# Kernel tuning notes

Measured on AMD Instinct MI355X. Metric: run time of the kernel, lower is better.

## Reference

```python
import jax, jax.numpy as jnp
import numpy as np

NQ = 10
C64 = jnp.complex64

# ---- gate matrices (built from traced fp32 params) ----

def u3(t, p, d):
    c = jnp.cos(t * 0.5).astype(C64)
    s = jnp.sin(t * 0.5).astype(C64)
    ep = jnp.exp(1j * p.astype(C64))
    ed = jnp.exp(1j * d.astype(C64))
    return jnp.stack([jnp.stack([c, -ed * s]), jnp.stack([ep * s, ep * ed * c])])

def ry(t):
    c = jnp.cos(t * 0.5).astype(C64)
    s = jnp.sin(t * 0.5).astype(C64)
    return jnp.stack([jnp.stack([c, -s]), jnp.stack([s, c])])

def rz(t):
    e = jnp.exp(-0.5j * t.astype(C64))
    ep = jnp.exp(0.5j * t.astype(C64))
    return jnp.diag(jnp.stack([e, ep]))

def rx(t):
    c = jnp.cos(t * 0.5).astype(C64)
    s = jnp.sin(t * 0.5).astype(C64)
    return jnp.stack([jnp.stack([c, -1j * s]), jnp.stack([-1j * s, c])])

def crz(t):
    one = jnp.ones((), C64)
    return jnp.diag(jnp.stack([one, one, jnp.exp(-0.5j * t.astype(C64)), jnp.exp(0.5j * t.astype(C64))]))

def crx(t):
    return jnp.eye(4, dtype=C64).at[2:, 2:].set(rx(t))

X = jnp.array([[0, 1], [1, 0]], dtype=C64)
CNOT = jnp.array([[1, 0, 0, 0], [0, 1, 0, 0], [0, 0, 0, 1], [0, 0, 1, 0]], dtype=C64)

# ---- gate application on state of shape (B, 2,...,2) ----

def ap1(st, U, w):
    ax = 1 + w
    s = jnp.moveaxis(st, ax, -1)
    s = s @ U.T
    return jnp.moveaxis(s, -1, ax)

def ap2(st, U, a, b):
    s = jnp.moveaxis(st, (1 + a, 1 + b), (-2, -1))
    sh = s.shape
    s = s.reshape(sh[:-2] + (4,)) @ U.T
    return jnp.moveaxis(s.reshape(sh), (-2, -1), (1 + a, 1 + b))

def conv_block(st, w, a, b):
    st = ap1(st, u3(w[0], w[1], w[2]), a)
    st = ap1(st, u3(w[3], w[4], w[5]), b)
    st = ap2(st, CNOT, a, b)
    st = ap1(st, ry(w[6]), a)
    st = ap1(st, rz(w[7]), b)
    st = ap2(st, CNOT, b, a)
    st = ap1(st, ry(w[8]), a)
    st = ap2(st, CNOT, a, b)
    st = ap1(st, u3(w[9], w[10], w[11]), a)
    st = ap1(st, u3(w[12], w[13], w[14]), b)
    return st

def pool_block(st, p, c, t):
    st = ap2(st, crz(p[0]), c, t)
    st = ap1(st, X, c)
    st = ap2(st, crx(p[1]), c, t)
    return st

def zexp(st, w):
    p = jnp.abs(st) ** 2  # fp32
    axes = tuple(ax for ax in range(1, NQ + 1) if ax != 1 + w)
    pz = p.sum(axis=axes)  # (B, 2)
    return pz[:, 0] - pz[:, 1]


def setup_inputs() -> dict:
    key = jax.random.key(0)
    ks = jax.random.split(key, 6)
    two_pi = 2.0 * np.pi
    return {
        "x": jax.random.normal(ks[0], (16384, 1024), dtype=jnp.float32),
        "weights_conv1": jax.random.uniform(ks[1], (10, 15), jnp.float32) * two_pi,
        "weights_conv2": jax.random.uniform(ks[2], (4, 15), jnp.float32) * two_pi,
        "weights_pool1": jax.random.uniform(ks[3], (5, 2), jnp.float32) * two_pi,
        "weights_pool2": jax.random.uniform(ks[4], (2, 2), jnp.float32) * two_pi,
        "weights_fc": jax.random.uniform(ks[5], (3,), jnp.float32) * two_pi,
    }


def reference(x, weights_conv1, weights_conv2, weights_pool1, weights_pool2, weights_fc):
    B = x.shape[0]
    # AmplitudeEmbedding with normalize=True (input already 1024-dim, no padding)
    nrm = jnp.linalg.norm(x, axis=1, keepdims=True)
    st = (x / nrm).astype(C64).reshape((B,) + (2,) * NQ)
    # conv layer 1: even pairs, odd pairs, wraparound (0, 9) reusing row 7
    for i in range(0, NQ, 2):
        st = conv_block(st, weights_conv1[i], i, i + 1)
    for i in range(1, NQ - 1, 2):
        st = conv_block(st, weights_conv1[i], i, i + 1)
    st = conv_block(st, weights_conv1[7], 0, NQ - 1)
    # pool layer 1
    for idx, i in enumerate(range(0, NQ, 2)):
        st = pool_block(st, weights_pool1[idx], i + 1, i)
    # conv layer 2 (stride-2 wires)
    for idx, i in enumerate(range(0, NQ - 2, 2)):
        st = conv_block(st, weights_conv2[idx], i, i + 2)
    # pool layer 2
    for idx, i in enumerate(range(0, NQ - 2, 4)):
        st = pool_block(st, weights_pool2[idx], i + 2, i)
    # fully-connected entanglers + RX rotations
    st = ap2(st, CNOT, 0, 4)
    st = ap2(st, CNOT, 2, 4)
    st = ap2(st, CNOT, 4, 0)
    st = ap1(st, rx(weights_fc[0]), 0)
    st = ap1(st, rx(weights_fc[1]), 2)
    st = ap1(st, rx(weights_fc[2]), 4)
    return jnp.stack([zexp(st, 0), zexp(st, 2)], axis=-1)  # (B, 2)
```

## Files before the change

kernel.cpp:

```cpp
#include <hip/hip_runtime.h>


typedef _Float16 f16;
typedef f16 f16x8 __attribute__((ext_vector_type(8)));
typedef f16 f16x4 __attribute__((ext_vector_type(4)));
typedef f16 f16x2 __attribute__((ext_vector_type(2)));
typedef float f32x4 __attribute__((ext_vector_type(4)));

__device__ inline float2 cmul(float2 a, float2 b) {
    return make_float2(a.x * b.x - a.y * b.y, a.x * b.y + a.y * b.x);
}
__device__ inline float2 cadd(float2 a, float2 b) {
    return make_float2(a.x + b.x, a.y + b.y);
}

struct M2 { float2 m[4]; };

__device__ inline M2 m2_u3(float t, float p, float d) {
    float c = cosf(0.5f * t), s = sinf(0.5f * t);
    float2 ep = make_float2(cosf(p), sinf(p));
    float2 ed = make_float2(cosf(d), sinf(d));
    M2 U;
    U.m[0] = make_float2(c, 0.f);
    U.m[1] = make_float2(-ed.x * s, -ed.y * s);
    U.m[2] = make_float2(ep.x * s, ep.y * s);
    float2 epd = cmul(ep, ed);
    U.m[3] = make_float2(epd.x * c, epd.y * c);
    return U;
}
__device__ inline M2 m2_ry(float t) {
    float c = cosf(0.5f * t), s = sinf(0.5f * t);
    M2 U;
    U.m[0] = make_float2(c, 0.f);  U.m[1] = make_float2(-s, 0.f);
    U.m[2] = make_float2(s, 0.f);  U.m[3] = make_float2(c, 0.f);
    return U;
}
__device__ inline M2 m2_rz(float t) {
    float c = cosf(0.5f * t), s = sinf(0.5f * t);
    M2 U;
    U.m[0] = make_float2(c, -s); U.m[1] = make_float2(0.f, 0.f);
    U.m[2] = make_float2(0.f, 0.f); U.m[3] = make_float2(c, s);
    return U;
}
__device__ inline M2 m2_rx(float t) {
    float c = cosf(0.5f * t), s = sinf(0.5f * t);
    M2 U;
    U.m[0] = make_float2(c, 0.f);   U.m[1] = make_float2(0.f, -s);
    U.m[2] = make_float2(0.f, -s);  U.m[3] = make_float2(c, 0.f);
    return U;
}

__device__ inline void ap2x2(float2& x, float2& y, const M2& U) {
    float2 nx = cadd(cmul(U.m[0], x), cmul(U.m[1], y));
    float2 ny = cadd(cmul(U.m[2], x), cmul(U.m[3], y));
    x = nx; y = ny;
}
__device__ inline void apA(float2 v[4], const M2& U) { ap2x2(v[0], v[2], U); ap2x2(v[1], v[3], U); }
__device__ inline void apB(float2 v[4], const M2& U) { ap2x2(v[0], v[1], U); ap2x2(v[2], v[3], U); }
__device__ inline void swapv(float2& a, float2& b) { float2 t = a; a = b; b = t; }

__device__ inline void conv_col(const float* w, float2 v[4]) {
    apA(v, m2_u3(w[0], w[1], w[2]));
    apB(v, m2_u3(w[3], w[4], w[5]));
    swapv(v[2], v[3]);
    apA(v, m2_ry(w[6]));
    apB(v, m2_rz(w[7]));
    swapv(v[1], v[3]);
    apA(v, m2_ry(w[8]));
    swapv(v[2], v[3]);
    apA(v, m2_u3(w[9], w[10], w[11]));
    apB(v, m2_u3(w[12], w[13], w[14]));
}
__device__ inline void pool_col(const float* p, float2 v[4]) {
    {
        float c = cosf(0.5f * p[0]), s = sinf(0.5f * p[0]);
        v[2] = cmul(v[2], make_float2(c, -s));
        v[3] = cmul(v[3], make_float2(c, s));
    }
    swapv(v[0], v[2]); swapv(v[1], v[3]);
    {
        M2 U = m2_rx(p[1]);
        ap2x2(v[2], v[3], U);
    }
}

__global__ void build_gates(const float* wc1, const float* wc2,
                            const float* wp1, const float* wp2,
                            const float* wfc, int2* gp, float2* gm) {
    const int t = threadIdx.x;
    const int n = t >> 2, c = t & 3;
    if (blockIdx.x != 0 || n >= 27) return;

    float2 v[4];
    for (int i = 0; i < 4; i++) v[i] = make_float2(0.f, 0.f);
    v[c] = make_float2(1.f, 0.f);

    int a, b;
    if (n < 5)        { int i = 2*n;       a = i;   b = i+1; conv_col(wc1 + 15*i, v); }
    else if (n < 9)   { int i = 2*(n-5)+1; a = i;   b = i+1; conv_col(wc1 + 15*i, v); }
    else if (n == 9)  { a = 0; b = 9;      conv_col(wc1 + 105, v); }
    else if (n < 15)  { int idx = n-10, i = 2*idx; a = i+1; b = i; pool_col(wp1 + 2*idx, v); }
    else if (n < 19)  { int idx = n-15, i = 2*idx; a = i; b = i+2; conv_col(wc2 + 15*idx, v); }
    else if (n == 19) { a = 2; b = 0;      pool_col(wp2 + 0, v); }
    else if (n == 20) { a = 6; b = 4;      pool_col(wp2 + 2, v); }
    else if (n <= 23) {
        a = (n == 21) ? 0 : (n == 22) ? 2 : 4;
        b = (n == 23) ? 0 : 4;
        swapv(v[2], v[3]);
    } else {
        a = (n == 24) ? 0 : (n == 25) ? 2 : 4;
        b = a + 1;
        apA(v, m2_rx(wfc[n - 24]));
    }
    if (c == 0) gp[n] = make_int2(9 - a, 9 - b);
    for (int i = 0; i < 4; i++) gm[n * 16 + i * 4 + c] = v[i];
}

#define SIM_BLOCKS 256
#define NORM_BLOCKS 2048

__global__ __launch_bounds__(256) void prep(const float* __restrict__ X,
                                            const int2* __restrict__ gp,
                                            const float2* __restrict__ gm,
                                            float* __restrict__ nrm2,
                                            f16* __restrict__ Xh,
                                            f16* __restrict__ BTh,
                                            float* __restrict__ out) {
    __shared__ float2 st[4][1025];
    const int bid = blockIdx.x;

    if (bid >= SIM_BLOCKS) {
        const int nb = bid - SIM_BLOCKS;
        const int w = threadIdx.x >> 6, l = threadIdx.x & 63;
        if (threadIdx.x < 16) out[nb * 16 + threadIdx.x] = 1.0f;
#pragma unroll
        for (int r = 0; r < 2; r++) {
            const int row = nb * 8 + w * 2 + r;
            const float4* xr = (const float4*)(X + (size_t)row * 1024);
            float s = 0.f;
#pragma unroll
            for (int ch = 0; ch < 4; ch++) {
                float4 v = xr[ch * 64 + l];
                f16x4 h;
                h[0] = (f16)v.x; h[1] = (f16)v.y; h[2] = (f16)v.z; h[3] = (f16)v.w;
                *(f16x4*)(Xh + (size_t)row * 1024 + (ch * 64 + l) * 4) = h;
                s += v.x * v.x + v.y * v.y + v.z * v.z + v.w * v.w;
            }
#pragma unroll
            for (int off = 32; off >= 1; off >>= 1) s += __shfl_xor(s, off, 64);
            if (l == 0) nrm2[row] = s;
        }
        return;
    }

    const int sb = bid;
    const int t0 = (sb & 7) * 128 + (sb >> 3) * 4;

    for (int i = threadIdx.x; i < 1024; i += 256) {
#pragma unroll
        for (int c = 0; c < 4; c++)
            st[c][i] = make_float2((i == t0 + c) ? 1.f : 0.f, 0.f);
    }
    __syncthreads();

    for (int g = 0; g < 27; g++) {
        const int2 p = gp[g];
        float2 m[16];
#pragma unroll
        for (int i = 0; i < 16; i++) m[i] = gm[g * 16 + i];
        const int p1 = p.x, p2 = p.y;
        const int lo = min(p1, p2), hi = max(p1, p2);
        const int q = threadIdx.x;
        const int m1 = (1 << lo) - 1;
        int tt = (q & m1) | ((q & ~m1) << 1);
        const int m2m = (1 << hi) - 1;
        const int i0 = (tt & m2m) | ((tt & ~m2m) << 1);
        int idx[4];
        for (int ga = 0; ga < 2; ga++)
            for (int gb = 0; gb < 2; gb++)
                idx[2 * ga + gb] = i0 | (ga << p1) | (gb << p2);
#pragma unroll
        for (int c = 0; c < 4; c++) {
            float2 v[4];
#pragma unroll
            for (int i = 0; i < 4; i++) v[i] = st[c][idx[i]];
#pragma unroll
            for (int i = 0; i < 4; i++) {
                float2 s = make_float2(0.f, 0.f);
#pragma unroll
                for (int j = 0; j < 4; j++) s = cadd(s, cmul(m[i * 4 + j], v[j]));
                st[c][idx[i]] = s;
            }
        }
        __syncthreads();
    }

    for (int s = threadIdx.x; s < 1024; s += 256) {
        const int b9 = (s >> 9) & 1, b7 = (s >> 7) & 1;
        if (b9 | b7) {
            const int grp = b9 ? b7 : 2;
            const int pos = (((s >> 8) & 1) << 7) | (s & 127);
            const int np = grp * 256 + pos;
            f16x4 re, im;
#pragma unroll
            for (int c = 0; c < 4; c++) {
                re[c] = (f16)st[c][s].x;
                im[c] = (f16)st[c][s].y;
            }
            *(f16x4*)(BTh + (size_t)np * 1024 + t0) = re;
            *(f16x4*)(BTh + (size_t)(np + 768) * 1024 + t0) = im;
        }
    }
}

__device__ __forceinline__ void glds16(const void* g, void* l) {
    __builtin_amdgcn_global_load_lds(
        (const __attribute__((address_space(1))) void*)g,
        (__attribute__((address_space(3))) void*)l, 16, 0, 0);
}

__global__ __launch_bounds__(256) void gemm_mfma(const f16* __restrict__ A,
                                                 const f16* __restrict__ Bt,
                                                 const float* __restrict__ nrm2,
                                                 float* __restrict__ out) {
    __shared__ char Ash[16384];
    __shared__ char Bsh[16384];
    const int tid = threadIdx.x;
    const int l = tid & 63, w = tid >> 6;
    const int wr = w >> 1, wc = w & 1;
    const int row0 = blockIdx.x * 128, col0 = blockIdx.y * 128;

    const int srow = l >> 3;
    const int kc = (l & 7) ^ (srow & 7);
    const f16* aS = A  + (size_t)(row0 + 32 * w + srow) * 1024 + kc * 8;
    const f16* bS = Bt + (size_t)(col0 + 32 * w + srow) * 1024 + kc * 8;
    char* aD = Ash + (32 * w) * 128;
    char* bD = Bsh + (32 * w) * 128;

    int aOff[4][2], bOff[4][2];
#pragma unroll
    for (int i = 0; i < 4; i++)
#pragma unroll
        for (int h = 0; h < 2; h++) {
            const int cphys = (((l >> 4) + 4 * h) ^ (l & 7));
            aOff[i][h] = (wr * 64 + i * 16 + (l & 15)) * 128 + cphys * 16;
            bOff[i][h] = (wc * 64 + i * 16 + (l & 15)) * 128 + cphys * 16;
        }

    f32x4 acc[4][4];
    const f32x4 z = {0.f, 0.f, 0.f, 0.f};
#pragma unroll
    for (int i = 0; i < 4; i++)
#pragma unroll
        for (int j = 0; j < 4; j++) acc[i][j] = z;

    for (int k0 = 0; k0 < 1024; k0 += 64) {
#pragma unroll
        for (int g = 0; g < 4; g++) {
            glds16(aS + k0 + g * 8 * 1024, aD + g * 1024);
            glds16(bS + k0 + g * 8 * 1024, bD + g * 1024);
        }
        __syncthreads();
#pragma unroll
        for (int h = 0; h < 2; h++) {
            f16x8 af[4], bf[4];
#pragma unroll
            for (int i = 0; i < 4; i++) {
                af[i] = *(const f16x8*)(Ash + aOff[i][h]);
                bf[i] = *(const f16x8*)(Bsh + bOff[i][h]);
            }
#pragma unroll
            for (int mi = 0; mi < 4; mi++)
#pragma unroll
                for (int ni = 0; ni < 4; ni++)
                    acc[mi][ni] = __builtin_amdgcn_mfma_f32_16x16x32_f16(
                        af[mi], bf[ni], acc[mi][ni], 0, 0, 0);
        }
        __syncthreads();
    }

    float c0[4][4], c1[4][4];
#pragma unroll
    for (int mi = 0; mi < 4; mi++)
#pragma unroll
        for (int rr = 0; rr < 4; rr++) { c0[mi][rr] = 0.f; c1[mi][rr] = 0.f; }
#pragma unroll
    for (int ni = 0; ni < 4; ni++) {
        const int n_glob = col0 + wc * 64 + ni * 16 + (l & 15);
        const int nm = (n_glob >= 768) ? n_glob - 768 : n_glob;
        const int grp = nm >> 8;
        const float w0 = (grp <= 1) ? 1.f : 0.f;
        const float w1 = (grp >= 1) ? 1.f : 0.f;
#pragma unroll
        for (int mi = 0; mi < 4; mi++)
#pragma unroll
            for (int rr = 0; rr < 4; rr++) {
                const float y = acc[mi][ni][rr];
                const float y2 = y * y;
                c0[mi][rr] += w0 * y2;
                c1[mi][rr] += w1 * y2;
            }
    }
#pragma unroll
    for (int off = 1; off < 16; off <<= 1)
#pragma unroll
        for (int mi = 0; mi < 4; mi++)
#pragma unroll
            for (int rr = 0; rr < 4; rr++) {
                c0[mi][rr] += __shfl_xor(c0[mi][rr], off, 64);
                c1[mi][rr] += __shfl_xor(c1[mi][rr], off, 64);
            }
    if ((l & 15) == 0) {
        const int q = l >> 4;
#pragma unroll
        for (int mi = 0; mi < 4; mi++)
#pragma unroll
            for (int rr = 0; rr < 4; rr++) {
                const int row = row0 + wr * 64 + mi * 16 + q * 4 + rr;
                const float inv = -2.0f / nrm2[row];
                atomicAdd(&out[row * 2 + 0], c0[mi][rr] * inv);
                atomicAdd(&out[row * 2 + 1], c1[mi][rr] * inv);
            }
    }
}

extern "C" void kernel_launch(void* const* d_in, const int* in_sizes, int n_in,
                              void* d_out, int out_size, void* d_ws, size_t ws_size,
                              hipStream_t stream) {
    const float* x   = (const float*)d_in[0];
    const float* wc1 = (const float*)d_in[1];
    const float* wc2 = (const float*)d_in[2];
    const float* wp1 = (const float*)d_in[3];
    const float* wp2 = (const float*)d_in[4];
    const float* wfc = (const float*)d_in[5];
    float* out = (float*)d_out;

    uintptr_t wsp = (uintptr_t)d_ws;
    int2*   gp     = (int2*)wsp;
    float2* gm     = (float2*)(wsp + 1024);
    f16*    BTh    = (f16*)(wsp + 8192);
    f16*    Xh     = (f16*)(wsp + 8192 + (3u << 20));
    float*  nrm2   = (float*)(wsp + 8192 + (35u << 20));

    build_gates<<<1, 128, 0, stream>>>(wc1, wc2, wp1, wp2, wfc, gp, gm);
    prep<<<SIM_BLOCKS + NORM_BLOCKS, 256, 0, stream>>>(x, gp, gm, nrm2, Xh, BTh, out);
    gemm_mfma<<<dim3(128, 12), 256, 0, stream>>>(Xh, BTh, nrm2, out);
}
```

Before: 221.7 us.

## Fuse gate construction into prep kernel and widen blocks to 512 threads

Removes the separate single-block build_gates launch. Each simulation block now computes the 27 gate matrices itself into shared memory and reads them from there, which saves a kernel launch and a dependent serial step. Blocks grow to 512 threads: simulation blocks split the four state columns across two thread halves, and norm blocks handle 16 rows instead of 8, so half as many norm blocks are launched. The cost is that all 256 simulation blocks repeat the gate-building work with transcendentals, and the larger blocks may reduce occupancy.

```diff
diff --git a/kernel.cpp b/kernel.cpp
--- a/kernel.cpp
+++ b/kernel.cpp
@@ -84,58 +84,32 @@
     }
 }
 
-__global__ void build_gates(const float* wc1, const float* wc2,
-                            const float* wp1, const float* wp2,
-                            const float* wfc, int2* gp, float2* gm) {
-    const int t = threadIdx.x;
-    const int n = t >> 2, c = t & 3;
-    if (blockIdx.x != 0 || n >= 27) return;
-
-    float2 v[4];
-    for (int i = 0; i < 4; i++) v[i] = make_float2(0.f, 0.f);
-    v[c] = make_float2(1.f, 0.f);
-
-    int a, b;
-    if (n < 5)        { int i = 2*n;       a = i;   b = i+1; conv_col(wc1 + 15*i, v); }
-    else if (n < 9)   { int i = 2*(n-5)+1; a = i;   b = i+1; conv_col(wc1 + 15*i, v); }
-    else if (n == 9)  { a = 0; b = 9;      conv_col(wc1 + 105, v); }
-    else if (n < 15)  { int idx = n-10, i = 2*idx; a = i+1; b = i; pool_col(wp1 + 2*idx, v); }
-    else if (n < 19)  { int idx = n-15, i = 2*idx; a = i; b = i+2; conv_col(wc2 + 15*idx, v); }
-    else if (n == 19) { a = 2; b = 0;      pool_col(wp2 + 0, v); }
-    else if (n == 20) { a = 6; b = 4;      pool_col(wp2 + 2, v); }
-    else if (n <= 23) {
-        a = (n == 21) ? 0 : (n == 22) ? 2 : 4;
-        b = (n == 23) ? 0 : 4;
-        swapv(v[2], v[3]);
-    } else {
-        a = (n == 24) ? 0 : (n == 25) ? 2 : 4;
-        b = a + 1;
-        apA(v, m2_rx(wfc[n - 24]));
-    }
-    if (c == 0) gp[n] = make_int2(9 - a, 9 - b);
-    for (int i = 0; i < 4; i++) gm[n * 16 + i * 4 + c] = v[i];
-}
-
 #define SIM_BLOCKS 256
-#define NORM_BLOCKS 2048
-
-__global__ __launch_bounds__(256) void prep(const float* __restrict__ X,
-                                            const int2* __restrict__ gp,
-                                            const float2* __restrict__ gm,
+#define NORM_BLOCKS 1024
+
+__global__ __launch_bounds__(512) void prep(const float* __restrict__ X,
+                                            const float* __restrict__ wc1,
+                                            const float* __restrict__ wc2,
+                                            const float* __restrict__ wp1,
+                                            const float* __restrict__ wp2,
+                                            const float* __restrict__ wfc,
                                             float* __restrict__ nrm2,
                                             f16* __restrict__ Xh,
                                             f16* __restrict__ BTh,
                                             float* __restrict__ out) {
     __shared__ float2 st[4][1025];
+    __shared__ float2 gmL[27 * 16];
+    __shared__ int2   gpL[27];
     const int bid = blockIdx.x;
+    const int tid = threadIdx.x;
 
     if (bid >= SIM_BLOCKS) {
         const int nb = bid - SIM_BLOCKS;
-        const int w = threadIdx.x >> 6, l = threadIdx.x & 63;
-        if (threadIdx.x < 16) out[nb * 16 + threadIdx.x] = 1.0f;
+        const int w = tid >> 6, l = tid & 63;
+        if (tid < 32) out[nb * 32 + tid] = 1.0f;
 #pragma unroll
         for (int r = 0; r < 2; r++) {
-            const int row = nb * 8 + w * 2 + r;
+            const int row = nb * 16 + w * 2 + r;
             const float4* xr = (const float4*)(X + (size_t)row * 1024);
             float s = 0.f;
 #pragma unroll
@@ -156,21 +130,49 @@
     const int sb = bid;
     const int t0 = (sb & 7) * 128 + (sb >> 3) * 4;
 
-    for (int i = threadIdx.x; i < 1024; i += 256) {
+    for (int i = tid; i < 1024; i += 512) {
 #pragma unroll
         for (int c = 0; c < 4; c++)
             st[c][i] = make_float2((i == t0 + c) ? 1.f : 0.f, 0.f);
     }
+
+    if (tid < 108) {
+        const int n = tid >> 2, c = tid & 3;
+        float2 v[4];
+        for (int i = 0; i < 4; i++) v[i] = make_float2(0.f, 0.f);
+        v[c] = make_float2(1.f, 0.f);
+
+        int a, b;
+        if (n < 5)        { int i = 2*n;       a = i;   b = i+1; conv_col(wc1 + 15*i, v); }
+        else if (n < 9)   { int i = 2*(n-5)+1; a = i;   b = i+1; conv_col(wc1 + 15*i, v); }
+        else if (n == 9)  { a = 0; b = 9;      conv_col(wc1 + 105, v); }
+        else if (n < 15)  { int idx = n-10, i = 2*idx; a = i+1; b = i; pool_col(wp1 + 2*idx, v); }
+        else if (n < 19)  { int idx = n-15, i = 2*idx; a = i; b = i+2; conv_col(wc2 + 15*idx, v); }
+        else if (n == 19) { a = 2; b = 0;      pool_col(wp2 + 0, v); }
+        else if (n == 20) { a = 6; b = 4;      pool_col(wp2 + 2, v); }
+        else if (n <= 23) {
+            a = (n == 21) ? 0 : (n == 22) ? 2 : 4;
+            b = (n == 23) ? 0 : 4;
+            swapv(v[2], v[3]);
+        } else {
+            a = (n == 24) ? 0 : (n == 25) ? 2 : 4;
+            b = a + 1;
+            apA(v, m2_rx(wfc[n - 24]));
+        }
+        if (c == 0) gpL[n] = make_int2(9 - a, 9 - b);
+        for (int i = 0; i < 4; i++) gmL[n * 16 + i * 4 + c] = v[i];
+    }
     __syncthreads();
 
+    const int cg = tid >> 8;
+    const int q = tid & 255;
     for (int g = 0; g < 27; g++) {
-        const int2 p = gp[g];
+        const int2 p = gpL[g];
         float2 m[16];
 #pragma unroll
-        for (int i = 0; i < 16; i++) m[i] = gm[g * 16 + i];
+        for (int i = 0; i < 16; i++) m[i] = gmL[g * 16 + i];
         const int p1 = p.x, p2 = p.y;
         const int lo = min(p1, p2), hi = max(p1, p2);
-        const int q = threadIdx.x;
         const int m1 = (1 << lo) - 1;
         int tt = (q & m1) | ((q & ~m1) << 1);
         const int m2m = (1 << hi) - 1;
@@ -180,7 +182,8 @@
             for (int gb = 0; gb < 2; gb++)
                 idx[2 * ga + gb] = i0 | (ga << p1) | (gb << p2);
 #pragma unroll
-        for (int c = 0; c < 4; c++) {
+        for (int cc = 0; cc < 2; cc++) {
+            const int c = 2 * cg + cc;
             float2 v[4];
 #pragma unroll
             for (int i = 0; i < 4; i++) v[i] = st[c][idx[i]];
@@ -195,7 +198,7 @@
         __syncthreads();
     }
 
-    for (int s = threadIdx.x; s < 1024; s += 256) {
+    for (int s = tid; s < 1024; s += 512) {
         const int b9 = (s >> 9) & 1, b7 = (s >> 7) & 1;
         if (b9 | b7) {
             const int grp = b9 ? b7 : 2;
@@ -336,13 +339,11 @@
     float* out = (float*)d_out;
 
     uintptr_t wsp = (uintptr_t)d_ws;
-    int2*   gp     = (int2*)wsp;
-    float2* gm     = (float2*)(wsp + 1024);
     f16*    BTh    = (f16*)(wsp + 8192);
     f16*    Xh     = (f16*)(wsp + 8192 + (3u << 20));
     float*  nrm2   = (float*)(wsp + 8192 + (35u << 20));
 
-    build_gates<<<1, 128, 0, stream>>>(wc1, wc2, wp1, wp2, wfc, gp, gm);
-    prep<<<SIM_BLOCKS + NORM_BLOCKS, 256, 0, stream>>>(x, gp, gm, nrm2, Xh, BTh, out);
+    prep<<<SIM_BLOCKS + NORM_BLOCKS, 512, 0, stream>>>(
+        x, wc1, wc2, wp1, wp2, wfc, nrm2, Xh, BTh, out);
     gemm_mfma<<<dim3(128, 12), 256, 0, stream>>>(Xh, BTh, nrm2, out);
 }
```

Result: no change. 221.0 us (-0.3%).
